# Kernel optimization log

Measured on AMD Instinct MI355X. Metric: run time of the kernel, lower is better.

Reference implementation:

```python
import jax, jax.numpy as jnp
import numpy as np

EPS = 1e-4

def setup_inputs() -> dict:
    key = jax.random.key(0)
    k1, k2 = jax.random.split(key)
    N, C, H, W = 64, 256, 56, 56
    x = jax.random.normal(k1, (N, C, H, W), dtype=jnp.float32)
    weight = jax.random.uniform(k2, (C, 1), dtype=jnp.float32)
    bias = jnp.zeros((C, 1), dtype=jnp.float32)
    return {"x": x, "weight": weight, "bias": bias}

def _zca_forward(x, weight, bias, groups=16):
    N, C, H, W = x.shape
    G = groups
    c = C // G  # per-group channel count
    M = N * H * W
    # [C, N*H*W], matching x.transpose(0,1).view(C, -1)
    xf = jnp.transpose(x, (1, 0, 2, 3)).reshape(C, M)
    mu = jnp.mean(xf, axis=1, keepdims=True)
    xc = xf - mu
    # Per-group covariance: the torch code builds the full CxC matrix and takes
    # diagonal blocks; computing only the blocks is the same math.
    xg = xc.reshape(G, c, M)
    cov = jnp.einsum('gim,gjm->gij', xg, xg) / M  # [G, c, c]
    cov = cov + EPS * jnp.eye(c, dtype=x.dtype)
    # torch.svd on a symmetric PSD matrix -> eigendecomposition; proj = V e^{-1/2} V^T
    e, v = jnp.linalg.eigh(cov)  # e: [G,c], v: [G,c,c]
    inv_sqrt = jax.lax.rsqrt(e)
    proj = jnp.einsum('gik,gk,gjk->gij', v, inv_sqrt, v)  # [G, c, c]
    xw = jnp.einsum('gij,gjm->gim', proj, xg).reshape(C, M)
    out = xw * weight + bias
    return jnp.transpose(out.reshape(C, N, H, W), (1, 0, 2, 3))

def reference(x, weight, bias):
    return _zca_forward(x, weight, bias)
```

## Files before the change

### kernel.cpp

```cpp
#include <hip/hip_runtime.h>
#include <math.h>

namespace {

constexpr int HW    = 56 * 56;
constexpr int NB    = 64;
constexpr int CTOT  = 256;
constexpr int CPG   = 16;
constexpr int GRP   = 16;
constexpr int MTOT  = NB * HW;
constexpr int NPAIR = 136;
constexpr int NACC  = CPG + NPAIR;
constexpr float EPSR = 1e-4f;
constexpr int BPG1  = 32;
constexpr int NS_IT = 14;
constexpr int TPOS  = 1024;
constexpr int TPS   = 4;

__host__ __device__ constexpr int pair_idx(int i, int j) {
    return i * CPG - (i * (i - 1)) / 2 + (j - i);
}

#define AS_GLOBAL(p) ((const __attribute__((address_space(1))) void*)(p))
#define AS_LOCAL(p)  ((__attribute__((address_space(3))) void*)(p))

__global__ __launch_bounds__(256, 2)
void cov_kernel(const float* __restrict__ x, float* __restrict__ accg) {
    const int g   = blockIdx.x / BPG1;
    const int b   = blockIdx.x % BPG1;
    const int tid = threadIdx.x;

    float sum[CPG];
    float acc[NPAIR];
#pragma unroll
    for (int i = 0; i < CPG; ++i) sum[i] = 0.f;
#pragma unroll
    for (int k = 0; k < NPAIR; ++k) acc[k] = 0.f;

    const int nchunk = MTOT / 4;
    const int stride = BPG1 * 256;
    for (int ch = b * 256 + tid; ch < nchunk; ch += stride) {
        const int m  = ch * 4;
        const int n  = m / HW;
        const int hw = m - n * HW;
        const float* p = x + (size_t)(n * CTOT + g * CPG) * HW + hw;
        float4 v[CPG];
#pragma unroll
        for (int j = 0; j < CPG; ++j)
            v[j] = *(const float4*)(p + (size_t)j * HW);
#pragma unroll
        for (int i = 0; i < CPG; ++i)
            sum[i] += (v[i].x + v[i].y) + (v[i].z + v[i].w);
#pragma unroll
        for (int i = 0; i < CPG; ++i)
#pragma unroll
            for (int j = i; j < CPG; ++j) {
                const int k = pair_idx(i, j);
                acc[k] = fmaf(v[i].x, v[j].x, acc[k]);
                acc[k] = fmaf(v[i].y, v[j].y, acc[k]);
                acc[k] = fmaf(v[i].z, v[j].z, acc[k]);
                acc[k] = fmaf(v[i].w, v[j].w, acc[k]);
            }
    }

#pragma unroll
    for (int i = 0; i < CPG; ++i) {
#pragma unroll
        for (int s = 32; s > 0; s >>= 1) sum[i] += __shfl_xor(sum[i], s, 64);
    }
#pragma unroll
    for (int k = 0; k < NPAIR; ++k) {
#pragma unroll
        for (int s = 32; s > 0; s >>= 1) acc[k] += __shfl_xor(acc[k], s, 64);
    }

    __shared__ float red[4][NACC];
    const int wave = tid >> 6;
    const int lane = tid & 63;
    if (lane == 0) {
#pragma unroll
        for (int i = 0; i < CPG; ++i) red[wave][i] = sum[i];
#pragma unroll
        for (int k = 0; k < NPAIR; ++k) red[wave][CPG + k] = acc[k];
    }
    __syncthreads();
    if (tid < NACC) {
        const float v = red[0][tid] + red[1][tid] + red[2][tid] + red[3][tid];
        atomicAdd(&accg[g * NACC + tid], v);
    }
}

__global__ __launch_bounds__(256, 1)
void ns_kernel(const float* __restrict__ accg,
               const float* __restrict__ weight, const float* __restrict__ bias,
               float* __restrict__ Pout, float* __restrict__ bfout) {
    __shared__ float A[CPG][CPG], Y[CPG][CPG], Z[CPG][CPG], T[CPG][CPG];
    __shared__ float mu[CPG];
    __shared__ float s_tr;
    const int g = blockIdx.x;
    const int t = threadIdx.x;
    const int i = t >> 4, j = t & 15;
    const float* a = accg + g * NACC;
    const float invM = 1.0f / (float)MTOT;

    if (t < CPG) mu[t] = a[t] * invM;
    __syncthreads();
    {
        const int lo = i < j ? i : j;
        const int hi = i < j ? j : i;
        float c = a[CPG + pair_idx(lo, hi)] * invM - mu[i] * mu[j];
        if (i == j) c += EPSR;
        A[i][j] = c;
    }
    __syncthreads();
    if (t == 0) {
        float tr = 0.f;
        for (int k = 0; k < CPG; ++k) tr += A[k][k];
        s_tr = tr;
    }
    __syncthreads();
    const float tr = s_tr;
    Y[i][j] = A[i][j] / tr;
    Z[i][j] = (i == j) ? 1.f : 0.f;
    __syncthreads();

    for (int it = 0; it < NS_IT; ++it) {
        float zy = 0.f;
#pragma unroll
        for (int k = 0; k < CPG; ++k) zy += Z[i][k] * Y[k][j];
        const float tij = ((i == j) ? 1.5f : 0.f) - 0.5f * zy;
        T[i][j] = tij;
        __syncthreads();
        float y2 = 0.f, z2 = 0.f;
#pragma unroll
        for (int k = 0; k < CPG; ++k) {
            y2 += Y[i][k] * T[k][j];
            z2 += T[i][k] * Z[k][j];
        }
        __syncthreads();
        Y[i][j] = y2;
        Z[i][j] = z2;
        __syncthreads();
    }

    const float pw = (Z[i][j] / sqrtf(tr)) * weight[g * CPG + i];
    Pout[g * 256 + t] = pw;

    T[i][j] = pw;
    __syncthreads();
    if (t < CPG) {
        float o = 0.f;
        for (int k = 0; k < CPG; ++k) o += T[t][k] * mu[k];
        bfout[g * CPG + t] = bias[g * CPG + t] - o;
    }
}

__global__ __launch_bounds__(256, 2)
void apply_kernel(const float* __restrict__ x, const float* __restrict__ Pg,
                  const float* __restrict__ bfg, float* __restrict__ out) {
    __shared__ __align__(16) float xs[CPG][TPOS];
    __shared__ float Pl[CPG][CPG];

    const int bid  = blockIdx.x;
    const int tile = bid & (TPS - 1);
    const int slab = bid >> 2;
    const int g    = slab & (GRP - 1);
    const int n    = slab >> 4;
    const int t    = threadIdx.x;
    const int lane = t & 63;
    const int w    = t >> 6;

    const int pos0 = tile * TPOS;
    const int npos = min(TPOS, HW - pos0);
    const float* xbase = x + ((size_t)n * CTOT + g * CPG) * HW + pos0;

    Pl[t >> 4][t & 15] = Pg[g * 256 + t];

#pragma unroll
    for (int jj = 0; jj < 4; ++jj) {
        const int j = w * 4 + jj;
        const float* src = xbase + (size_t)j * HW;
#pragma unroll
        for (int q = 0; q < 4; ++q) {
            const int f = q * 64 + lane;
            if (4 * f < npos) {
                __builtin_amdgcn_global_load_lds(AS_GLOBAL(src + 4 * f),
                                                 AS_LOCAL(&xs[j][q * 256]),
                                                 16, 0, 0);
            }
        }
    }
    __syncthreads();

    const int i0 = w * 4;
    float4 acc[4][4];
#pragma unroll
    for (int ii = 0; ii < 4; ++ii)
#pragma unroll
        for (int q = 0; q < 4; ++q) acc[ii][q] = make_float4(0.f, 0.f, 0.f, 0.f);

#pragma unroll
    for (int j = 0; j < CPG; ++j) {
        float4 xv[4];
#pragma unroll
        for (int q = 0; q < 4; ++q)
            xv[q] = *(const float4*)&xs[j][4 * (q * 64 + lane)];
        float p[4];
#pragma unroll
        for (int ii = 0; ii < 4; ++ii) p[ii] = Pl[i0 + ii][j];
#pragma unroll
        for (int ii = 0; ii < 4; ++ii)
#pragma unroll
            for (int q = 0; q < 4; ++q) {
                acc[ii][q].x = fmaf(p[ii], xv[q].x, acc[ii][q].x);
                acc[ii][q].y = fmaf(p[ii], xv[q].y, acc[ii][q].y);
                acc[ii][q].z = fmaf(p[ii], xv[q].z, acc[ii][q].z);
                acc[ii][q].w = fmaf(p[ii], xv[q].w, acc[ii][q].w);
            }
    }

#pragma unroll
    for (int ii = 0; ii < 4; ++ii) {
        const int i = i0 + ii;
        const float bb = bfg[g * CPG + i];
        float* po = out + ((size_t)n * CTOT + g * CPG + i) * HW + pos0;
#pragma unroll
        for (int q = 0; q < 4; ++q) {
            const int f = q * 64 + lane;
            if (4 * f < npos) {
                float4 r;
                r.x = acc[ii][q].x + bb;
                r.y = acc[ii][q].y + bb;
                r.z = acc[ii][q].z + bb;
                r.w = acc[ii][q].w + bb;
                *(float4*)(po + 4 * f) = r;
            }
        }
    }
}

}

extern "C" void kernel_launch(void* const* d_in, const int* in_sizes, int n_in,
                              void* d_out, int out_size, void* d_ws, size_t ws_size,
                              hipStream_t stream) {
    const float* x      = (const float*)d_in[0];
    const float* weight = (const float*)d_in[1];
    const float* bias   = (const float*)d_in[2];
    float* out = (float*)d_out;
    float* ws  = (float*)d_ws;

    float* acc = ws;
    float* Pw  = ws + 2560;
    float* bf  = ws + 6656;

    hipMemsetAsync(acc, 0, GRP * NACC * sizeof(float), stream);

    cov_kernel<<<GRP * BPG1, 256, 0, stream>>>(x, acc);
    ns_kernel<<<GRP, 256, 0, stream>>>(acc, weight, bias, Pw, bf);
    apply_kernel<<<NB * GRP * TPS, 256, 0, stream>>>(x, Pw, bf, out);
}
```

Measured before the change: 795.6 us.

## Prefetch scalar loads in covariance loop and restructure apply kernel to register-only tiles

The covariance kernel changes from float4 loads with 4x FMA per pair to scalar per-position loads, with a software-pipelined prefetch of the next iteration's 16 channel values. The apply kernel drops the LDS staging via global_load_lds and has each thread load all 16 channels for a float4 position, then compute all 16 outputs in registers from a transposed P matrix stored in shared memory. The apply kernel also drops spatial tiling, so it launches one block per (n, group) slab. Scalar loads in the covariance pass cut memory-level parallelism per thread. The apply kernel's 128 live float4 registers may lower occupancy.

```diff
diff --git a/kernel.cpp b/kernel.cpp
--- a/kernel.cpp
+++ b/kernel.cpp
@@ -14,15 +14,11 @@
 constexpr float EPSR = 1e-4f;
 constexpr int BPG1  = 32;
 constexpr int NS_IT = 14;
-constexpr int TPOS  = 1024;
-constexpr int TPS   = 4;
+constexpr int F4    = HW / 4;
 
 __host__ __device__ constexpr int pair_idx(int i, int j) {
     return i * CPG - (i * (i - 1)) / 2 + (j - i);
 }
-
-#define AS_GLOBAL(p) ((const __attribute__((address_space(1))) void*)(p))
-#define AS_LOCAL(p)  ((__attribute__((address_space(3))) void*)(p))
 
 __global__ __launch_bounds__(256, 2)
 void cov_kernel(const float* __restrict__ x, float* __restrict__ accg) {
@@ -37,30 +33,39 @@
 #pragma unroll
     for (int k = 0; k < NPAIR; ++k) acc[k] = 0.f;
 
-    const int nchunk = MTOT / 4;
     const int stride = BPG1 * 256;
-    for (int ch = b * 256 + tid; ch < nchunk; ch += stride) {
-        const int m  = ch * 4;
+
+    float v[CPG], vn[CPG];
+    int m = b * 256 + tid;
+    {
         const int n  = m / HW;
         const int hw = m - n * HW;
-        const float* p = x + (size_t)(n * CTOT + g * CPG) * HW + hw;
-        float4 v[CPG];
-#pragma unroll
-        for (int j = 0; j < CPG; ++j)
-            v[j] = *(const float4*)(p + (size_t)j * HW);
-#pragma unroll
-        for (int i = 0; i < CPG; ++i)
-            sum[i] += (v[i].x + v[i].y) + (v[i].z + v[i].w);
-#pragma unroll
-        for (int i = 0; i < CPG; ++i)
-#pragma unroll
-            for (int j = i; j < CPG; ++j) {
-                const int k = pair_idx(i, j);
-                acc[k] = fmaf(v[i].x, v[j].x, acc[k]);
-                acc[k] = fmaf(v[i].y, v[j].y, acc[k]);
-                acc[k] = fmaf(v[i].z, v[j].z, acc[k]);
-                acc[k] = fmaf(v[i].w, v[j].w, acc[k]);
-            }
+        const float* p = x + ((size_t)n * CTOT + (size_t)g * CPG) * HW + hw;
+#pragma unroll
+        for (int j = 0; j < CPG; ++j) v[j] = p[(size_t)j * HW];
+    }
+
+    while (true) {
+        const int mn = m + stride;
+        const bool more = (mn < MTOT);
+        if (more) {
+            const int n  = mn / HW;
+            const int hw = mn - n * HW;
+            const float* p = x + ((size_t)n * CTOT + (size_t)g * CPG) * HW + hw;
+#pragma unroll
+            for (int j = 0; j < CPG; ++j) vn[j] = p[(size_t)j * HW];
+        }
+#pragma unroll
+        for (int i = 0; i < CPG; ++i) {
+            sum[i] += v[i];
+#pragma unroll
+            for (int j = i; j < CPG; ++j)
+                acc[pair_idx(i, j)] = fmaf(v[i], v[j], acc[pair_idx(i, j)]);
+        }
+        if (!more) break;
+        m = mn;
+#pragma unroll
+        for (int j = 0; j < CPG; ++j) v[j] = vn[j];
     }
 
 #pragma unroll
@@ -85,8 +90,8 @@
     }
     __syncthreads();
     if (tid < NACC) {
-        const float v = red[0][tid] + red[1][tid] + red[2][tid] + red[3][tid];
-        atomicAdd(&accg[g * NACC + tid], v);
+        const float v0 = red[0][tid] + red[1][tid] + red[2][tid] + red[3][tid];
+        atomicAdd(&accg[g * NACC + tid], v0);
     }
 }
 
@@ -144,7 +149,7 @@
     }
 
     const float pw = (Z[i][j] / sqrtf(tr)) * weight[g * CPG + i];
-    Pout[g * 256 + t] = pw;
+    Pout[g * 256 + j * CPG + i] = pw;
 
     T[i][j] = pw;
     __syncthreads();
@@ -158,84 +163,66 @@
 __global__ __launch_bounds__(256, 2)
 void apply_kernel(const float* __restrict__ x, const float* __restrict__ Pg,
                   const float* __restrict__ bfg, float* __restrict__ out) {
-    __shared__ __align__(16) float xs[CPG][TPOS];
-    __shared__ float Pl[CPG][CPG];
-
-    const int bid  = blockIdx.x;
-    const int tile = bid & (TPS - 1);
-    const int slab = bid >> 2;
+    __shared__ float Pl[CPG * CPG];
+    __shared__ float bl[CPG];
+
+    const int slab = blockIdx.x;
     const int g    = slab & (GRP - 1);
     const int n    = slab >> 4;
     const int t    = threadIdx.x;
-    const int lane = t & 63;
-    const int w    = t >> 6;
-
-    const int pos0 = tile * TPOS;
-    const int npos = min(TPOS, HW - pos0);
-    const float* xbase = x + ((size_t)n * CTOT + g * CPG) * HW + pos0;
-
-    Pl[t >> 4][t & 15] = Pg[g * 256 + t];
-
-#pragma unroll
-    for (int jj = 0; jj < 4; ++jj) {
-        const int j = w * 4 + jj;
-        const float* src = xbase + (size_t)j * HW;
-#pragma unroll
-        for (int q = 0; q < 4; ++q) {
-            const int f = q * 64 + lane;
-            if (4 * f < npos) {
-                __builtin_amdgcn_global_load_lds(AS_GLOBAL(src + 4 * f),
-                                                 AS_LOCAL(&xs[j][q * 256]),
-                                                 16, 0, 0);
+
+    Pl[t] = Pg[g * 256 + t];
+    if (t < CPG) bl[t] = bfg[g * CPG + t];
+    __syncthreads();
+
+    const size_t base = ((size_t)n * CTOT + (size_t)g * CPG) * HW;
+    const float* xb = x + base;
+    float*       ob = out + base;
+
+    for (int f = t; f < F4; f += 256) {
+        const float* px = xb + 4 * f;
+        float4 xv[CPG];
+#pragma unroll
+        for (int j = 0; j < CPG; ++j)
+            xv[j] = *(const float4*)(px + j * HW);
+
+        float4 acc[CPG];
+#pragma unroll
+        for (int i = 0; i < CPG; ++i) {
+            const float bb = bl[i];
+            acc[i] = make_float4(bb, bb, bb, bb);
+        }
+
+#pragma unroll
+        for (int j = 0; j < CPG; ++j) {
+            const float4* prow = (const float4*)&Pl[j * CPG];
+            const float4 p0 = prow[0], p1 = prow[1], p2 = prow[2], p3 = prow[3];
+            const float4 xj = xv[j];
+#pragma unroll
+            for (int q = 0; q < 4; ++q) {
+                const float4 pq = (q == 0) ? p0 : (q == 1) ? p1 : (q == 2) ? p2 : p3;
+                acc[q * 4 + 0].x = fmaf(pq.x, xj.x, acc[q * 4 + 0].x);
+                acc[q * 4 + 0].y = fmaf(pq.x, xj.y, acc[q * 4 + 0].y);
+                acc[q * 4 + 0].z = fmaf(pq.x, xj.z, acc[q * 4 + 0].z);
+                acc[q * 4 + 0].w = fmaf(pq.x, xj.w, acc[q * 4 + 0].w);
+                acc[q * 4 + 1].x = fmaf(pq.y, xj.x, acc[q * 4 + 1].x);
+                acc[q * 4 + 1].y = fmaf(pq.y, xj.y, acc[q * 4 + 1].y);
+                acc[q * 4 + 1].z = fmaf(pq.y, xj.z, acc[q * 4 + 1].z);
+                acc[q * 4 + 1].w = fmaf(pq.y, xj.w, acc[q * 4 + 1].w);
+                acc[q * 4 + 2].x = fmaf(pq.z, xj.x, acc[q * 4 + 2].x);
+                acc[q * 4 + 2].y = fmaf(pq.z, xj.y, acc[q * 4 + 2].y);
+                acc[q * 4 + 2].z = fmaf(pq.z, xj.z, acc[q * 4 + 2].z);
+                acc[q * 4 + 2].w = fmaf(pq.z, xj.w, acc[q * 4 + 2].w);
+                acc[q * 4 + 3].x = fmaf(pq.w, xj.x, acc[q * 4 + 3].x);
+                acc[q * 4 + 3].y = fmaf(pq.w, xj.y, acc[q * 4 + 3].y);
+                acc[q * 4 + 3].z = fmaf(pq.w, xj.z, acc[q * 4 + 3].z);
+                acc[q * 4 + 3].w = fmaf(pq.w, xj.w, acc[q * 4 + 3].w);
             }
         }
-    }
-    __syncthreads();
-
-    const int i0 = w * 4;
-    float4 acc[4][4];
-#pragma unroll
-    for (int ii = 0; ii < 4; ++ii)
-#pragma unroll
-        for (int q = 0; q < 4; ++q) acc[ii][q] = make_float4(0.f, 0.f, 0.f, 0.f);
-
-#pragma unroll
-    for (int j = 0; j < CPG; ++j) {
-        float4 xv[4];
-#pragma unroll
-        for (int q = 0; q < 4; ++q)
-            xv[q] = *(const float4*)&xs[j][4 * (q * 64 + lane)];
-        float p[4];
-#pragma unroll
-        for (int ii = 0; ii < 4; ++ii) p[ii] = Pl[i0 + ii][j];
-#pragma unroll
-        for (int ii = 0; ii < 4; ++ii)
-#pragma unroll
-            for (int q = 0; q < 4; ++q) {
-                acc[ii][q].x = fmaf(p[ii], xv[q].x, acc[ii][q].x);
-                acc[ii][q].y = fmaf(p[ii], xv[q].y, acc[ii][q].y);
-                acc[ii][q].z = fmaf(p[ii], xv[q].z, acc[ii][q].z);
-                acc[ii][q].w = fmaf(p[ii], xv[q].w, acc[ii][q].w);
-            }
-    }
-
-#pragma unroll
-    for (int ii = 0; ii < 4; ++ii) {
-        const int i = i0 + ii;
-        const float bb = bfg[g * CPG + i];
-        float* po = out + ((size_t)n * CTOT + g * CPG + i) * HW + pos0;
-#pragma unroll
-        for (int q = 0; q < 4; ++q) {
-            const int f = q * 64 + lane;
-            if (4 * f < npos) {
-                float4 r;
-                r.x = acc[ii][q].x + bb;
-                r.y = acc[ii][q].y + bb;
-                r.z = acc[ii][q].z + bb;
-                r.w = acc[ii][q].w + bb;
-                *(float4*)(po + 4 * f) = r;
-            }
-        }
+
+#pragma unroll
+        for (int i = 0; i < CPG; ++i)
+            *(float4*)(ob + i * HW + 4 * f) = acc[i];
     }
 }
 
@@ -258,5 +245,5 @@
 
     cov_kernel<<<GRP * BPG1, 256, 0, stream>>>(x, acc);
     ns_kernel<<<GRP, 256, 0, stream>>>(acc, weight, bias, Pw, bf);
-    apply_kernel<<<NB * GRP * TPS, 256, 0, stream>>>(x, Pw, bf, out);
-}
+    apply_kernel<<<NB * GRP, 256, 0, stream>>>(x, Pw, bf, out);
+}
```

New measurement: 953.5 us. 1.2x slower.
